# Kernel tuning notes

Hardware: AMD Instinct MI355X
Metric: run time of the kernel (lower is better)

## Reference

```python
import jax, jax.numpy as jnp
import numpy as np

EPS = 1e-6
NUM_HEADS = 12

def _rms(x, w):
    return x * jax.lax.rsqrt(jnp.mean(x * x, axis=-1, keepdims=True) + EPS) * w

def _ln(x, w=None, b=None):
    m = jnp.mean(x, axis=-1, keepdims=True)
    v = jnp.mean((x - m) ** 2, axis=-1, keepdims=True)
    y = (x - m) * jax.lax.rsqrt(v + EPS)
    return y * w + b if w is not None else y

def _rope(x, cos, sin):
    # x: [B,T,H,hd]; cos/sin: [T,hd//2]; adjacent pairs form complex numbers
    B, T, H, hd = x.shape
    xp = x.reshape(B, T, H, hd // 2, 2)
    xr, xi = xp[..., 0], xp[..., 1]
    c = cos[None, :, None, :]
    s = sin[None, :, None, :]
    yr = xr * c - xi * s
    yi = xr * s + xi * c
    return jnp.stack([yr, yi], axis=-1).reshape(B, T, H, hd)

def _attn(q, k, v, mask=None):
    # q: [B,Tq,H,hd], k/v: [B,Tk,H,hd]
    scale = 1.0 / np.sqrt(q.shape[-1]).astype(np.float32)
    s = jnp.einsum('bqhd,bkhd->bhqk', q, k) * scale
    if mask is not None:
        s = jnp.where(mask, s, jnp.asarray(-1e30, s.dtype))
    p = jax.nn.softmax(s, axis=-1)
    return jnp.einsum('bhqk,bkhd->bqhd', p, v)

def _forward(x, context, t_mod, freqs_cos, freqs_sin,
             sa_wq, sa_bq, sa_wk, sa_bk, sa_wv, sa_bv, sa_wo, sa_bo, sa_nq, sa_nk,
             ca_wq, ca_bq, ca_wk, ca_bk, ca_wv, ca_bv, ca_wo, ca_bo, ca_nq, ca_nk,
             norm3_w, norm3_b, ffn_w1, ffn_b1, ffn_w2, ffn_b2, modulation, num_frames):
    B, T, D = x.shape
    F = num_frames
    S = T // F
    H = NUM_HEADS
    hd = D // H
    # adaLN modulation: modulation [1,6,D] broadcast-added to t_mod [B,F,6,D]
    mod = modulation[:, None] + t_mod
    sh_msa, sc_msa, g_msa, sh_mlp, sc_mlp, g_mlp = [mod[:, :, i] for i in range(6)]
    # ---- causal self-attention with RoPE ----
    nx = _ln(x).reshape(B, F, S, D)
    inp = (nx * (1.0 + sc_msa[:, :, None]) + sh_msa[:, :, None]).reshape(B, T, D)
    q = _rms(inp @ sa_wq + sa_bq, sa_nq).reshape(B, T, H, hd)
    k = _rms(inp @ sa_wk + sa_bk, sa_nk).reshape(B, T, H, hd)
    v = (inp @ sa_wv + sa_bv).reshape(B, T, H, hd)
    rq = _rope(q, freqs_cos, freqs_sin)
    rk = _rope(k, freqs_cos, freqs_sin)
    frame_id = jnp.arange(T) // S
    mask = (frame_id[None, :] <= frame_id[:, None])[None, None]  # block-causal by frame
    y = _attn(rq, rk, v, mask).reshape(B, T, D) @ sa_wo + sa_bo
    x = x + (y.reshape(B, F, S, D) * g_msa[:, :, None]).reshape(B, T, D)
    # ---- cross-attention (no image branch) ----
    xn = _ln(x, norm3_w, norm3_b)
    Tc = context.shape[1]
    q = _rms(xn @ ca_wq + ca_bq, ca_nq).reshape(B, T, H, hd)
    k = _rms(context @ ca_wk + ca_bk, ca_nk).reshape(B, Tc, H, hd)
    v = (context @ ca_wv + ca_bv).reshape(B, Tc, H, hd)
    y = _attn(q, k, v).reshape(B, T, D) @ ca_wo + ca_bo
    x = x + y
    # ---- FFN with modulation ----
    nx = _ln(x).reshape(B, F, S, D)
    inp = (nx * (1.0 + sc_mlp[:, :, None]) + sh_mlp[:, :, None]).reshape(B, T, D)
    h = jax.nn.gelu(inp @ ffn_w1 + ffn_b1, approximate=True)
    y = h @ ffn_w2 + ffn_b2
    x = x + (y.reshape(B, F, S, D) * g_mlp[:, :, None]).reshape(B, T, D)
    return x

def setup_inputs() -> dict:
    key = jax.random.key(0)
    B, F, S, D, FF, Tc = 1, 6, 512, 1536, 8960, 512
    T = F * S
    hd = D // NUM_HEADS
    ks = iter(jax.random.split(key, 48))
    def rn(shape, std=1.0):
        return jax.random.normal(next(ks), shape, dtype=jnp.float32) * std
    pos = jnp.arange(T, dtype=jnp.float32)
    inv = 1.0 / (10000.0 ** (jnp.arange(hd // 2, dtype=jnp.float32) / (hd // 2)))
    ang = pos[:, None] * inv[None, :]
    inp = {
        'x': rn((B, T, D)),
        'context': rn((B, Tc, D)),
        't_mod': rn((B, F, 6, D), 0.1),
        'freqs_cos': jnp.cos(ang),
        'freqs_sin': jnp.sin(ang),
    }
    w = 0.02
    for p in ['sa', 'ca']:
        inp[p + '_wq'] = rn((D, D), w); inp[p + '_bq'] = jnp.zeros((D,), jnp.float32)
        inp[p + '_wk'] = rn((D, D), w); inp[p + '_bk'] = jnp.zeros((D,), jnp.float32)
        inp[p + '_wv'] = rn((D, D), w); inp[p + '_bv'] = jnp.zeros((D,), jnp.float32)
        inp[p + '_wo'] = rn((D, D), w); inp[p + '_bo'] = jnp.zeros((D,), jnp.float32)
        inp[p + '_nq'] = jnp.ones((D,), jnp.float32)
        inp[p + '_nk'] = jnp.ones((D,), jnp.float32)
    inp['norm3_w'] = jnp.ones((D,), jnp.float32)
    inp['norm3_b'] = jnp.zeros((D,), jnp.float32)
    inp['ffn_w1'] = rn((D, FF), w); inp['ffn_b1'] = jnp.zeros((FF,), jnp.float32)
    inp['ffn_w2'] = rn((FF, D), w); inp['ffn_b2'] = jnp.zeros((D,), jnp.float32)
    inp['modulation'] = rn((1, 6, D), 1.0 / np.sqrt(D))
    inp['num_frames'] = F
    return inp

def reference(x, context, t_mod, freqs_cos, freqs_sin,
              sa_wq, sa_bq, sa_wk, sa_bk, sa_wv, sa_bv, sa_wo, sa_bo, sa_nq, sa_nk,
              ca_wq, ca_bq, ca_wk, ca_bk, ca_wv, ca_bv, ca_wo, ca_bo, ca_nq, ca_nk,
              norm3_w, norm3_b, ffn_w1, ffn_b1, ffn_w2, ffn_b2, modulation, num_frames):
    return _forward(x, context, t_mod, freqs_cos, freqs_sin,
                    sa_wq, sa_bq, sa_wk, sa_bk, sa_wv, sa_bv, sa_wo, sa_bo, sa_nq, sa_nk,
                    ca_wq, ca_bq, ca_wk, ca_bk, ca_wv, ca_bv, ca_wo, ca_bo, ca_nq, ca_nk,
                    norm3_w, norm3_b, ffn_w1, ffn_b1, ffn_w2, ffn_b2, modulation, num_frames)
```

## Files before the change

kernel.cpp:

```cpp
#include <hip/hip_runtime.h>
#include <cmath>

#define DEV __device__ __forceinline__

constexpr int T_TOK   = 3072;
constexpr int D_MODEL = 1536;
constexpr int FRAMES  = 6;
constexpr int NH      = 12;
constexpr int HD      = 128;
constexpr int FF_DIM  = 8960;
constexpr int TC      = 512;
constexpr float EPS_F = 1e-6f;
constexpr float ATT_SCALE = 0.08838834764831845f;

typedef short bf16x8 __attribute__((ext_vector_type(8)));
typedef float f32x4  __attribute__((ext_vector_type(4)));

DEV ushort f2bf(float f) {
  unsigned u = __builtin_bit_cast(unsigned, f);
  unsigned r = u + 0x7fff + ((u >> 16) & 1);
  return (ushort)(r >> 16);
}

DEV void gload16(const void* g, void* l) {
  __builtin_amdgcn_global_load_lds(
      (const __attribute__((address_space(1))) void*)g,
      (__attribute__((address_space(3))) void*)l, 16, 0, 0);
}

__global__ __launch_bounds__(256) void mod_kernel(
    const float* __restrict__ modulation, const float* __restrict__ t_mod,
    float* __restrict__ modbuf) {
  int i = blockIdx.x * 256 + threadIdx.x;
  if (i >= FRAMES * 6 * D_MODEL) return;
  int d  = i % D_MODEL;
  int mi = (i / D_MODEL) % 6;
  modbuf[i] = modulation[mi * D_MODEL + d] + t_mod[i];
}

__global__ __launch_bounds__(256) void cvt_bf16_kernel(
    const float* __restrict__ in, ushort* __restrict__ out, int n4) {
  int i = blockIdx.x * 256 + threadIdx.x;
  if (i >= n4) return;
  float4 v = ((const float4*)in)[i];
  ushort4 o;
  o.x = f2bf(v.x); o.y = f2bf(v.y); o.z = f2bf(v.z); o.w = f2bf(v.w);
  ((ushort4*)out)[i] = o;
}

__global__ __launch_bounds__(256) void wconv_kernel(
    const float* __restrict__ W, ushort* __restrict__ Wt, int K, int N) {
  __shared__ float tile[64][65];
  const int k0 = blockIdx.y * 64, n0 = blockIdx.x * 64;
  const int t = threadIdx.x;
  const int r = t >> 4, c4 = (t & 15) * 4;
#pragma unroll
  for (int i = 0; i < 4; ++i) {
    float4 v = *(const float4*)&W[(long)(k0 + r + 16 * i) * N + n0 + c4];
    tile[r + 16 * i][c4 + 0] = v.x; tile[r + 16 * i][c4 + 1] = v.y;
    tile[r + 16 * i][c4 + 2] = v.z; tile[r + 16 * i][c4 + 3] = v.w;
  }
  __syncthreads();
  const int orow = t >> 5, oc2 = (t & 31) * 2;
#pragma unroll
  for (int j = 0; j < 8; ++j) {
    int nrow = orow + 8 * j;
    ushort2 o;
    o.x = f2bf(tile[oc2][nrow]);
    o.y = f2bf(tile[oc2 + 1][nrow]);
    *(ushort2*)&Wt[(long)(n0 + nrow) * K + k0 + oc2] = o;
  }
}

__global__ __launch_bounds__(256) void vtrans_kernel(
    const float* __restrict__ V, int stride, int Tv, ushort* __restrict__ Vt) {
  __shared__ float tile[64][65];
  const int t0 = blockIdx.x * 64, d0 = blockIdx.y * 64;
  const int t = threadIdx.x;
  const int r = t >> 4, c4 = (t & 15) * 4;
#pragma unroll
  for (int i = 0; i < 4; ++i) {
    float4 v = *(const float4*)&V[(long)(t0 + r + 16 * i) * stride + d0 + c4];
    tile[r + 16 * i][c4 + 0] = v.x; tile[r + 16 * i][c4 + 1] = v.y;
    tile[r + 16 * i][c4 + 2] = v.z; tile[r + 16 * i][c4 + 3] = v.w;
  }
  __syncthreads();
  const int od = t >> 2, tc = (t & 3) * 16;
#pragma unroll
  for (int j4 = 0; j4 < 4; ++j4) {
    ushort4 o;
    o.x = f2bf(tile[tc + j4 * 4 + 0][od]);
    o.y = f2bf(tile[tc + j4 * 4 + 1][od]);
    o.z = f2bf(tile[tc + j4 * 4 + 2][od]);
    o.w = f2bf(tile[tc + j4 * 4 + 3][od]);
    *(ushort4*)&Vt[(long)(d0 + od) * Tv + t0 + tc + j4 * 4] = o;
  }
}

DEV void block_reduce2(float& s, float& s2, float* red, int t) {
  int lane = t & 63, w = t >> 6;
#pragma unroll
  for (int o = 32; o > 0; o >>= 1) {
    s  += __shfl_down(s,  o, 64);
    s2 += __shfl_down(s2, o, 64);
  }
  if (lane == 0) { red[w] = s; red[4 + w] = s2; }
  __syncthreads();
  s  = (red[0] + red[1]) + (red[2] + red[3]);
  s2 = (red[4] + red[5]) + (red[6] + red[7]);
}

__global__ __launch_bounds__(256) void ln_mod_kernel(
    const float* __restrict__ x, const float* __restrict__ modbuf,
    int ish, int isc, ushort* __restrict__ out) {
  __shared__ float red[8];
  int row = blockIdx.x, t = threadIdx.x;
  const float* xr = x + (long)row * D_MODEL;
  float vals[6];
  float s = 0.f, s2 = 0.f;
#pragma unroll
  for (int i = 0; i < 6; ++i) {
    float v = xr[t + 256 * i];
    vals[i] = v; s += v; s2 += v * v;
  }
  block_reduce2(s, s2, red, t);
  float mean = s * (1.f / D_MODEL);
  float var  = s2 * (1.f / D_MODEL) - mean * mean;
  float rs   = 1.f / sqrtf(var + EPS_F);
  const float* mb = modbuf + (long)(row >> 9) * 6 * D_MODEL;
#pragma unroll
  for (int i = 0; i < 6; ++i) {
    int d = t + 256 * i;
    float y = (vals[i] - mean) * rs;
    out[(long)row * D_MODEL + d] = f2bf(y * (1.f + mb[isc * D_MODEL + d]) + mb[ish * D_MODEL + d]);
  }
}

__global__ __launch_bounds__(256) void ln_affine_kernel(
    const float* __restrict__ x, const float* __restrict__ w,
    const float* __restrict__ b, ushort* __restrict__ out) {
  __shared__ float red[8];
  int row = blockIdx.x, t = threadIdx.x;
  const float* xr = x + (long)row * D_MODEL;
  float vals[6];
  float s = 0.f, s2 = 0.f;
#pragma unroll
  for (int i = 0; i < 6; ++i) {
    float v = xr[t + 256 * i];
    vals[i] = v; s += v; s2 += v * v;
  }
  block_reduce2(s, s2, red, t);
  float mean = s * (1.f / D_MODEL);
  float var  = s2 * (1.f / D_MODEL) - mean * mean;
  float rs   = 1.f / sqrtf(var + EPS_F);
#pragma unroll
  for (int i = 0; i < 6; ++i) {
    int d = t + 256 * i;
    float y = (vals[i] - mean) * rs;
    out[(long)row * D_MODEL + d] = f2bf(y * w[d] + b[d]);
  }
}

template <bool ROPE>
__global__ __launch_bounds__(256) void rmsbf_kernel(
    const float* __restrict__ in, int stride, const float* __restrict__ w,
    const float* __restrict__ cosb, const float* __restrict__ sinb,
    ushort* __restrict__ out) {
  __shared__ float red[8];
  int row = blockIdx.x, t = threadIdx.x;
  const float* xr = in + (long)row * stride;
  float vals[6];
  float s2 = 0.f, dummy = 0.f;
#pragma unroll
  for (int i = 0; i < 6; ++i) {
    float v = xr[t + 256 * i];
    vals[i] = v; s2 += v * v;
  }
  block_reduce2(s2, dummy, red, t);
  float rs = 1.f / sqrtf(s2 * (1.f / D_MODEL) + EPS_F);
  ushort* orow = out + (long)row * D_MODEL;
  if (ROPE) {
#pragma unroll
    for (int pi = 0; pi < 3; ++pi) {
      int p = t + 256 * pi;
      int hh = p >> 6, ii = p & 63;
      int d0 = hh * HD + 2 * ii;
      float a = xr[d0] * rs * w[d0];
      float b = xr[d0 + 1] * rs * w[d0 + 1];
      float c = cosb[(long)row * 64 + ii];
      float sn = sinb[(long)row * 64 + ii];
      ushort2 o;
      o.x = f2bf(a * c - b * sn);
      o.y = f2bf(a * sn + b * c);
      *(ushort2*)&orow[d0] = o;
    }
  } else {
#pragma unroll
    for (int i = 0; i < 6; ++i) {
      int d = t + 256 * i;
      orow[d] = f2bf(vals[i] * rs * w[d]);
    }
  }
}

template <int EPI>
__global__ __launch_bounds__(256) void mgemm_kernel(
    const ushort* __restrict__ A, const ushort* __restrict__ Bt,
    const float* __restrict__ bias, const float* __restrict__ res,
    const float* __restrict__ modbuf, int gidx,
    void* __restrict__ Cout, int M, int N, int K, int ldc) {
  __shared__ ushort As[128 * 32];
  __shared__ ushort Bs[128 * 32];
  const int t = threadIdx.x;
  const int bm = blockIdx.y * 128, bn = blockIdx.x * 128;
  const int wave = t >> 6, lane = t & 63;
  const int wr = (wave >> 1) * 64, wc = (wave & 1) * 64;
  const int l15 = lane & 15, l4 = lane >> 4;

  f32x4 acc[4][4] = {};

  const int srow  = t >> 2;
  const int skoff = (t & 3) * 8;
  const ushort* Ag = A  + (long)(bm + srow) * K + skoff;
  const ushort* Bg = Bt + (long)(bn + srow) * K + skoff;
  ushort* Asl = As + t * 8;
  ushort* Bsl = Bs + t * 8;
  const long half = (long)64 * K;

  for (int k0 = 0; k0 < K; k0 += 32) {
    __syncthreads();
    gload16(Ag + k0, Asl);
    gload16(Ag + k0 + half, Asl + 2048);
    gload16(Bg + k0, Bsl);
    gload16(Bg + k0 + half, Bsl + 2048);
    asm volatile("s_waitcnt vmcnt(0)" ::: "memory");
    __syncthreads();
    bf16x8 af[4], bfr[4];
#pragma unroll
    for (int m = 0; m < 4; ++m)
      af[m] = *(const bf16x8*)&As[(wr + m * 16 + l15) * 32 + l4 * 8];
#pragma unroll
    for (int n = 0; n < 4; ++n)
      bfr[n] = *(const bf16x8*)&Bs[(wc + n * 16 + l15) * 32 + l4 * 8];
#pragma unroll
    for (int m = 0; m < 4; ++m)
#pragma unroll
      for (int n = 0; n < 4; ++n)
        acc[m][n] = __builtin_amdgcn_mfma_f32_16x16x32_bf16(af[m], bfr[n], acc[m][n], 0, 0, 0);
  }

#pragma unroll
  for (int m = 0; m < 4; ++m) {
#pragma unroll
    for (int r = 0; r < 4; ++r) {
      const int grow = bm + wr + m * 16 + l4 * 4 + r;
      const long rowoff = (long)grow * ldc;
      const float* mrow = nullptr;
      if (EPI == 2) mrow = modbuf + (long)((grow >> 9) * 6 + gidx) * D_MODEL;
#pragma unroll
      for (int n = 0; n < 4; ++n) {
        const int gcol = bn + wc + n * 16 + l15;
        float val = acc[m][n][r] + bias[gcol];
        if (EPI == 0) {
          ((float*)Cout)[rowoff + gcol] = val;
        } else if (EPI == 1) {
          float u = val;
          val = u / (1.f + __expf(-1.5957691216057308f * (u + 0.044715f * u * u * u)));
          ((ushort*)Cout)[rowoff + gcol] = f2bf(val);
        } else if (EPI == 2) {
          ((float*)Cout)[rowoff + gcol] = res[rowoff + gcol] + val * mrow[gcol];
        } else {
          ((float*)Cout)[rowoff + gcol] = res[rowoff + gcol] + val;
        }
      }
    }
  }
}

template <bool CAUSAL>
__global__ __launch_bounds__(256) void mattn_kernel(
    const ushort* __restrict__ Qb, const ushort* __restrict__ Kb,
    const ushort* __restrict__ Vt, ushort* __restrict__ O, int Tk) {
  __shared__ ushort Kl[64 * 136];
  __shared__ ushort Vl[128 * 72];
  __shared__ ushort Pl[4][32 * 72];
  const int t = threadIdx.x;
  const int h = blockIdx.y;
  const int qb = CAUSAL ? (gridDim.x - 1 - blockIdx.x) : blockIdx.x;
  const int q0 = qb * 128;
  const int wave = t >> 6, lane = t & 63;
  const int l15 = lane & 15, l4 = lane >> 4;
  const int wq = wave * 32;
  const int kmax = CAUSAL ? (((q0 >> 9) + 1) << 9) : Tk;

  bf16x8 qf[2][4];
#pragma unroll
  for (int mf = 0; mf < 2; ++mf)
#pragma unroll
    for (int ks = 0; ks < 4; ++ks)
      qf[mf][ks] = *(const bf16x8*)&Qb[(long)(q0 + wq + mf * 16 + l15) * D_MODEL + h * HD + ks * 32 + l4 * 8];

  f32x4 ao[2][8] = {};
  float m_run[8], l_run[8];
#pragma unroll
  for (int i = 0; i < 8; ++i) { m_run[i] = -1e30f; l_run[i] = 0.f; }

  const ushort* Vh = Vt + (long)h * HD * Tk;
  ushort* Plw = &Pl[wave][0];

  for (int k0 = 0; k0 < kmax; k0 += 64) {
    __syncthreads();
    {
      const int r = t >> 2, c0 = (t & 3) * 8;
      const ushort* src = Kb + (long)(k0 + r) * D_MODEL + h * HD + c0;
#pragma unroll
      for (int j = 0; j < 4; ++j)
        *(bf16x8*)&Kl[r * 136 + c0 + j * 32] = *(const bf16x8*)&src[j * 32];
    }
    {
      const int d = t >> 1, c0 = (t & 1) * 32;
      const ushort* src = Vh + (long)d * Tk + k0 + c0;
#pragma unroll
      for (int j = 0; j < 4; ++j)
        *(bf16x8*)&Vl[d * 72 + c0 + j * 8] = *(const bf16x8*)&src[j * 8];
    }
    __syncthreads();

    f32x4 s[2][4] = {};
#pragma unroll
    for (int n = 0; n < 4; ++n) {
      bf16x8 kf[4];
#pragma unroll
      for (int ks = 0; ks < 4; ++ks)
        kf[ks] = *(const bf16x8*)&Kl[(n * 16 + l15) * 136 + ks * 32 + l4 * 8];
#pragma unroll
      for (int mf = 0; mf < 2; ++mf)
#pragma unroll
        for (int ks = 0; ks < 4; ++ks)
          s[mf][n] = __builtin_amdgcn_mfma_f32_16x16x32_bf16(qf[mf][ks], kf[ks], s[mf][n], 0, 0, 0);
    }

#pragma unroll
    for (int mf = 0; mf < 2; ++mf) {
      float mx[4], al[4], ps[4];
#pragma unroll
      for (int r = 0; r < 4; ++r)
        mx[r] = fmaxf(fmaxf(s[mf][0][r], s[mf][1][r]), fmaxf(s[mf][2][r], s[mf][3][r])) * ATT_SCALE;
#pragma unroll
      for (int off = 1; off < 16; off <<= 1)
#pragma unroll
        for (int r = 0; r < 4; ++r)
          mx[r] = fmaxf(mx[r], __shfl_xor(mx[r], off, 64));
#pragma unroll
      for (int r = 0; r < 4; ++r) {
        const int idx = mf * 4 + r;
        float mnew = fmaxf(m_run[idx], mx[r]);
        al[r] = __expf(m_run[idx] - mnew);
        m_run[idx] = mnew;
        float p0 = __expf(s[mf][0][r] * ATT_SCALE - mnew);
        float p1 = __expf(s[mf][1][r] * ATT_SCALE - mnew);
        float p2 = __expf(s[mf][2][r] * ATT_SCALE - mnew);
        float p3 = __expf(s[mf][3][r] * ATT_SCALE - mnew);
        s[mf][0][r] = p0; s[mf][1][r] = p1; s[mf][2][r] = p2; s[mf][3][r] = p3;
        ps[r] = (p0 + p1) + (p2 + p3);
      }
#pragma unroll
      for (int off = 1; off < 16; off <<= 1)
#pragma unroll
        for (int r = 0; r < 4; ++r)
          ps[r] += __shfl_xor(ps[r], off, 64);
#pragma unroll
      for (int r = 0; r < 4; ++r)
        l_run[mf * 4 + r] = l_run[mf * 4 + r] * al[r] + ps[r];
#pragma unroll
      for (int nd = 0; nd < 8; ++nd)
#pragma unroll
        for (int r = 0; r < 4; ++r)
          ao[mf][nd][r] *= al[r];
#pragma unroll
      for (int n = 0; n < 4; ++n)
#pragma unroll
        for (int r = 0; r < 4; ++r)
          Plw[(mf * 16 + l4 * 4 + r) * 72 + n * 16 + l15] = f2bf(s[mf][n][r]);
    }

#pragma unroll
    for (int ks2 = 0; ks2 < 2; ++ks2) {
      bf16x8 paf[2];
#pragma unroll
      for (int mf = 0; mf < 2; ++mf)
        paf[mf] = *(const bf16x8*)&Plw[(mf * 16 + l15) * 72 + ks2 * 32 + l4 * 8];
#pragma unroll
      for (int nd = 0; nd < 8; ++nd) {
        bf16x8 vf = *(const bf16x8*)&Vl[(nd * 16 + l15) * 72 + ks2 * 32 + l4 * 8];
#pragma unroll
        for (int mf = 0; mf < 2; ++mf)
          ao[mf][nd] = __builtin_amdgcn_mfma_f32_16x16x32_bf16(paf[mf], vf, ao[mf][nd], 0, 0, 0);
      }
    }
  }

#pragma unroll
  for (int mf = 0; mf < 2; ++mf)
#pragma unroll
    for (int r = 0; r < 4; ++r) {
      float inv = 1.f / l_run[mf * 4 + r];
      long rb = (long)(q0 + wq + mf * 16 + l4 * 4 + r) * D_MODEL + h * HD + l15;
#pragma unroll
      for (int nd = 0; nd < 8; ++nd)
        O[rb + nd * 16] = f2bf(ao[mf][nd][r] * inv);
    }
}

extern "C" void kernel_launch(void* const* d_in, const int* in_sizes, int n_in,
                              void* d_out, int out_size, void* d_ws, size_t ws_size,
                              hipStream_t stream) {
  const float* x      = (const float*)d_in[0];
  const float* ctx    = (const float*)d_in[1];
  const float* t_mod  = (const float*)d_in[2];
  const float* fcos   = (const float*)d_in[3];
  const float* fsin   = (const float*)d_in[4];
  const float* sa_wq = (const float*)d_in[5];  const float* sa_bq = (const float*)d_in[6];
  const float* sa_wk = (const float*)d_in[7];  const float* sa_bk = (const float*)d_in[8];
  const float* sa_wv = (const float*)d_in[9];  const float* sa_bv = (const float*)d_in[10];
  const float* sa_wo = (const float*)d_in[11]; const float* sa_bo = (const float*)d_in[12];
  const float* sa_nq = (const float*)d_in[13]; const float* sa_nk = (const float*)d_in[14];
  const float* ca_wq = (const float*)d_in[15]; const float* ca_bq = (const float*)d_in[16];
  const float* ca_wk = (const float*)d_in[17]; const float* ca_bk = (const float*)d_in[18];
  const float* ca_wv = (const float*)d_in[19]; const float* ca_bv = (const float*)d_in[20];
  const float* ca_wo = (const float*)d_in[21]; const float* ca_bo = (const float*)d_in[22];
  const float* ca_nq = (const float*)d_in[23]; const float* ca_nk = (const float*)d_in[24];
  const float* n3w = (const float*)d_in[25]; const float* n3b = (const float*)d_in[26];
  const float* w1 = (const float*)d_in[27]; const float* b1 = (const float*)d_in[28];
  const float* w2 = (const float*)d_in[29]; const float* b2 = (const float*)d_in[30];
  const float* modulation = (const float*)d_in[31];
  (void)in_sizes; (void)n_in; (void)out_size; (void)ws_size;

  float* out = (float*)d_out;
  char*  wsb = (char*)d_ws;

  float*  modbuf  = (float*)(wsb + 0);
  float*  biascat = (float*)(wsb + 221184);
  ushort* wscr    = (ushort*)(wsb + 251904);
  ushort* inp     = (ushort*)(wsb + 27777024);
  char*   R       = wsb + 37214208;
  ushort* attb    = (ushort*)(wsb + 93837312);
  ushort* Qbb     = (ushort*)(wsb + 103274496);
  char*   KV      = wsb + 112711680;
  char*   M       = wsb + 131586048;

  float*  qkvb = (float*)R;
  float*  qc   = (float*)R;
  float*  kvc  = (float*)(R + 18874368);
  ushort* hb   = (ushort*)R;
  ushort* Kbb  = (ushort*)KV;
  ushort* Vtb  = (ushort*)(KV + 9437184);
  float*  x1   = (float*)KV;
  ushort* ctxb = (ushort*)M;
  ushort* Kbc  = (ushort*)M;
  ushort* Vtc  = (ushort*)(M + 1572864);

  dim3 b256(256);
  dim3 gT(T_TOK);
  dim3 gattn(T_TOK / 128, NH);
  const long WQ = (long)D_MODEL * D_MODEL;

  mod_kernel<<<dim3((FRAMES * 6 * D_MODEL + 255) / 256), b256, 0, stream>>>(modulation, t_mod, modbuf);
  hipMemcpyAsync(biascat + 0,    sa_bq, 6144, hipMemcpyDeviceToDevice, stream);
  hipMemcpyAsync(biascat + 1536, sa_bk, 6144, hipMemcpyDeviceToDevice, stream);
  hipMemcpyAsync(biascat + 3072, sa_bv, 6144, hipMemcpyDeviceToDevice, stream);
  hipMemcpyAsync(biascat + 4608, ca_bk, 6144, hipMemcpyDeviceToDevice, stream);
  hipMemcpyAsync(biascat + 6144, ca_bv, 6144, hipMemcpyDeviceToDevice, stream);
  cvt_bf16_kernel<<<dim3(TC * D_MODEL / 4 / 256), b256, 0, stream>>>(ctx, ctxb, TC * D_MODEL / 4);

  dim3 gw(D_MODEL / 64, D_MODEL / 64);

  ln_mod_kernel<<<gT, b256, 0, stream>>>(x, modbuf, 0, 1, inp);
  wconv_kernel<<<gw, b256, 0, stream>>>(sa_wq, wscr + 0 * WQ, D_MODEL, D_MODEL);
  wconv_kernel<<<gw, b256, 0, stream>>>(sa_wk, wscr + 1 * WQ, D_MODEL, D_MODEL);
  wconv_kernel<<<gw, b256, 0, stream>>>(sa_wv, wscr + 2 * WQ, D_MODEL, D_MODEL);
  mgemm_kernel<0><<<dim3(4608 / 128, T_TOK / 128), b256, 0, stream>>>(
      inp, wscr, biascat, nullptr, nullptr, 0, qkvb, T_TOK, 4608, D_MODEL, 4608);
  rmsbf_kernel<true><<<gT, b256, 0, stream>>>(qkvb, 4608, sa_nq, fcos, fsin, Qbb);
  rmsbf_kernel<true><<<gT, b256, 0, stream>>>(qkvb + 1536, 4608, sa_nk, fcos, fsin, Kbb);
  vtrans_kernel<<<dim3(T_TOK / 64, D_MODEL / 64), b256, 0, stream>>>(qkvb + 3072, 4608, T_TOK, Vtb);
  mattn_kernel<true><<<gattn, b256, 0, stream>>>(Qbb, Kbb, Vtb, attb, T_TOK);
  wconv_kernel<<<gw, b256, 0, stream>>>(sa_wo, wscr, D_MODEL, D_MODEL);
  mgemm_kernel<2><<<dim3(D_MODEL / 128, T_TOK / 128), b256, 0, stream>>>(
      attb, wscr, sa_bo, x, modbuf, 2, x1, T_TOK, D_MODEL, D_MODEL, D_MODEL);

  ln_affine_kernel<<<gT, b256, 0, stream>>>(x1, n3w, n3b, inp);
  wconv_kernel<<<gw, b256, 0, stream>>>(ca_wq, wscr, D_MODEL, D_MODEL);
  mgemm_kernel<0><<<dim3(D_MODEL / 128, T_TOK / 128), b256, 0, stream>>>(
      inp, wscr, ca_bq, nullptr, nullptr, 0, qc, T_TOK, D_MODEL, D_MODEL, D_MODEL);
  rmsbf_kernel<false><<<gT, b256, 0, stream>>>(qc, 1536, ca_nq, nullptr, nullptr, Qbb);
  wconv_kernel<<<gw, b256, 0, stream>>>(ca_wk, wscr + 0 * WQ, D_MODEL, D_MODEL);
  wconv_kernel<<<gw, b256, 0, stream>>>(ca_wv, wscr + 1 * WQ, D_MODEL, D_MODEL);
  mgemm_kernel<0><<<dim3(3072 / 128, TC / 128), b256, 0, stream>>>(
      ctxb, wscr, biascat + 4608, nullptr, nullptr, 0, kvc, TC, 3072, D_MODEL, 3072);
  rmsbf_kernel<false><<<dim3(TC), b256, 0, stream>>>(kvc, 3072, ca_nk, nullptr, nullptr, Kbc);
  vtrans_kernel<<<dim3(TC / 64, D_MODEL / 64), b256, 0, stream>>>(kvc + 1536, 3072, TC, Vtc);
  mattn_kernel<false><<<gattn, b256, 0, stream>>>(Qbb, Kbc, Vtc, attb, TC);
  wconv_kernel<<<gw, b256, 0, stream>>>(ca_wo, wscr, D_MODEL, D_MODEL);
  mgemm_kernel<3><<<dim3(D_MODEL / 128, T_TOK / 128), b256, 0, stream>>>(
      attb, wscr, ca_bo, x1, nullptr, 0, x1, T_TOK, D_MODEL, D_MODEL, D_MODEL);

  ln_mod_kernel<<<gT, b256, 0, stream>>>(x1, modbuf, 3, 4, inp);
  wconv_kernel<<<dim3(FF_DIM / 64, D_MODEL / 64), b256, 0, stream>>>(w1, wscr, D_MODEL, FF_DIM);
  mgemm_kernel<1><<<dim3(FF_DIM / 128, T_TOK / 128), b256, 0, stream>>>(
      inp, wscr, b1, nullptr, nullptr, 0, hb, T_TOK, FF_DIM, D_MODEL, FF_DIM);
  wconv_kernel<<<dim3(D_MODEL / 64, FF_DIM / 64), b256, 0, stream>>>(w2, wscr, FF_DIM, D_MODEL);
  mgemm_kernel<2><<<dim3(D_MODEL / 128, T_TOK / 128), b256, 0, stream>>>(
      hb, wscr, b2, x1, modbuf, 5, out, T_TOK, D_MODEL, FF_DIM, D_MODEL);
}
```

Baseline: 1.235 ms.

## Load attention K/V fragments straight from global and transpose score tile

The attention kernel no longer stages K and V tiles in shared memory behind block barriers. Each wave now loads its K and V MFMA fragments directly from global memory into registers. The score MFMA is computed as K·Q, so each lane holds one query row: the row max and row sum need only two cross-lane shuffles, and the scale is folded into exp2. The 2D grid becomes a 1D grid with a remap intended to spread heads and query blocks across XCDs. The trade-off is that all four waves now fetch the same K/V tiles, which multiplies L2 traffic and raises register pressure.

```diff
diff --git a/kernel.cpp b/kernel.cpp
--- a/kernel.cpp
+++ b/kernel.cpp
@@ -20,6 +20,10 @@
   unsigned u = __builtin_bit_cast(unsigned, f);
   unsigned r = u + 0x7fff + ((u >> 16) & 1);
   return (ushort)(r >> 16);
+}
+
+DEV unsigned packbf2(float lo, float hi) {
+  return (unsigned)f2bf(lo) | ((unsigned)f2bf(hi) << 16);
 }
 
 DEV void gload16(const void* g, void* l) {
@@ -281,17 +285,17 @@
 __global__ __launch_bounds__(256) void mattn_kernel(
     const ushort* __restrict__ Qb, const ushort* __restrict__ Kb,
     const ushort* __restrict__ Vt, ushort* __restrict__ O, int Tk) {
-  __shared__ ushort Kl[64 * 136];
-  __shared__ ushort Vl[128 * 72];
   __shared__ ushort Pl[4][32 * 72];
   const int t = threadIdx.x;
-  const int h = blockIdx.y;
-  const int qb = CAUSAL ? (gridDim.x - 1 - blockIdx.x) : blockIdx.x;
-  const int q0 = qb * 128;
-  const int wave = t >> 6, lane = t & 63;
-  const int l15 = lane & 15, l4 = lane >> 4;
+  const int bid = blockIdx.x;
+  const int L = (bid & 7) * 36 + (bid >> 3);
+  const int h  = L / 24;
+  const int q0 = (23 - (L % 24)) * 128;
+  const int wave = t >> 6;
+  const int l15 = t & 15, l4 = (t >> 4) & 3;
   const int wq = wave * 32;
   const int kmax = CAUSAL ? (((q0 >> 9) + 1) << 9) : Tk;
+  const float SC2 = ATT_SCALE * 1.4426950408889634f;
 
   bf16x8 qf[2][4];
 #pragma unroll
@@ -301,115 +305,105 @@
       qf[mf][ks] = *(const bf16x8*)&Qb[(long)(q0 + wq + mf * 16 + l15) * D_MODEL + h * HD + ks * 32 + l4 * 8];
 
   f32x4 ao[2][8] = {};
-  float m_run[8], l_run[8];
-#pragma unroll
-  for (int i = 0; i < 8; ++i) { m_run[i] = -1e30f; l_run[i] = 0.f; }
-
+  float m_run[2] = {-1e30f, -1e30f};
+  float l_run[2] = {0.f, 0.f};
+
+  const ushort* Kh = Kb + h * HD;
   const ushort* Vh = Vt + (long)h * HD * Tk;
-  ushort* Plw = &Pl[wave][0];
+  ushort*   Plw   = &Pl[wave][0];
+  unsigned* Plw32 = (unsigned*)Plw;
 
   for (int k0 = 0; k0 < kmax; k0 += 64) {
-    __syncthreads();
-    {
-      const int r = t >> 2, c0 = (t & 3) * 8;
-      const ushort* src = Kb + (long)(k0 + r) * D_MODEL + h * HD + c0;
-#pragma unroll
-      for (int j = 0; j < 4; ++j)
-        *(bf16x8*)&Kl[r * 136 + c0 + j * 32] = *(const bf16x8*)&src[j * 32];
+    bf16x8 kf[4][4];
+#pragma unroll
+    for (int n = 0; n < 4; ++n)
+#pragma unroll
+      for (int ks = 0; ks < 4; ++ks)
+        kf[n][ks] = *(const bf16x8*)&Kh[(long)(k0 + n * 16 + l15) * D_MODEL + ks * 32 + l4 * 8];
+
+    f32x4 s[2][4] = {};
+#pragma unroll
+    for (int n = 0; n < 4; ++n)
+#pragma unroll
+      for (int mf = 0; mf < 2; ++mf)
+#pragma unroll
+        for (int ks = 0; ks < 4; ++ks)
+          s[mf][n] = __builtin_amdgcn_mfma_f32_16x16x32_bf16(kf[n][ks], qf[mf][ks], s[mf][n], 0, 0, 0);
+
+    bf16x8 vf[8][2];
+#pragma unroll
+    for (int nd = 0; nd < 8; ++nd)
+#pragma unroll
+      for (int ks2 = 0; ks2 < 2; ++ks2)
+        vf[nd][ks2] = *(const bf16x8*)&Vh[(long)(nd * 16 + l15) * Tk + k0 + ks2 * 32 + l4 * 8];
+
+#pragma unroll
+    for (int mf = 0; mf < 2; ++mf) {
+      float mx = s[mf][0][0];
+#pragma unroll
+      for (int n = 0; n < 4; ++n)
+#pragma unroll
+        for (int r = 0; r < 4; ++r) mx = fmaxf(mx, s[mf][n][r]);
+      mx *= SC2;
+      mx = fmaxf(mx, __shfl_xor(mx, 16, 64));
+      mx = fmaxf(mx, __shfl_xor(mx, 32, 64));
+      float mnew = fmaxf(m_run[mf], mx);
+      float al = exp2f(m_run[mf] - mnew);
+      m_run[mf] = mnew;
+      float p[4][4];
+      float ps = 0.f;
+#pragma unroll
+      for (int n = 0; n < 4; ++n)
+#pragma unroll
+        for (int r = 0; r < 4; ++r) {
+          p[n][r] = exp2f(s[mf][n][r] * SC2 - mnew);
+          ps += p[n][r];
+        }
+      ps += __shfl_xor(ps, 16, 64);
+      ps += __shfl_xor(ps, 32, 64);
+      l_run[mf] = l_run[mf] * al + ps;
+#pragma unroll
+      for (int n = 0; n < 4; ++n) {
+        uint2 wv;
+        wv.x = packbf2(p[n][0], p[n][1]);
+        wv.y = packbf2(p[n][2], p[n][3]);
+        *(uint2*)&Plw32[(mf * 16 + l15) * 36 + n * 8 + l4 * 2] = wv;
+      }
+      float alq[4];
+#pragma unroll
+      for (int r = 0; r < 4; ++r) alq[r] = __shfl(al, l4 * 4 + r, 64);
+#pragma unroll
+      for (int nd = 0; nd < 8; ++nd)
+#pragma unroll
+        for (int r = 0; r < 4; ++r) ao[mf][nd][r] *= alq[r];
     }
-    {
-      const int d = t >> 1, c0 = (t & 1) * 32;
-      const ushort* src = Vh + (long)d * Tk + k0 + c0;
-#pragma unroll
-      for (int j = 0; j < 4; ++j)
-        *(bf16x8*)&Vl[d * 72 + c0 + j * 8] = *(const bf16x8*)&src[j * 8];
+
+    bf16x8 paf[2][2];
+#pragma unroll
+    for (int mf = 0; mf < 2; ++mf)
+#pragma unroll
+      for (int ks2 = 0; ks2 < 2; ++ks2)
+        paf[mf][ks2] = *(const bf16x8*)&Plw[(mf * 16 + l15) * 72 + ks2 * 32 + l4 * 8];
+#pragma unroll
+    for (int nd = 0; nd < 8; ++nd)
+#pragma unroll
+      for (int ks2 = 0; ks2 < 2; ++ks2)
+#pragma unroll
+        for (int mf = 0; mf < 2; ++mf)
+          ao[mf][nd] = __builtin_amdgcn_mfma_f32_16x16x32_bf16(paf[mf][ks2], vf[nd][ks2], ao[mf][nd], 0, 0, 0);
+  }
+
+#pragma unroll
+  for (int mf = 0; mf < 2; ++mf) {
+#pragma unroll
+    for (int r = 0; r < 4; ++r) {
+      float linv = 1.f / __shfl(l_run[mf], l4 * 4 + r, 64);
+      long rb = (long)(q0 + wq + mf * 16 + l4 * 4 + r) * D_MODEL + h * HD + l15;
+#pragma unroll
+      for (int nd = 0; nd < 8; ++nd)
+        O[rb + nd * 16] = f2bf(ao[mf][nd][r] * linv);
     }
-    __syncthreads();
-
-    f32x4 s[2][4] = {};
-#pragma unroll
-    for (int n = 0; n < 4; ++n) {
-      bf16x8 kf[4];
-#pragma unroll
-      for (int ks = 0; ks < 4; ++ks)
-        kf[ks] = *(const bf16x8*)&Kl[(n * 16 + l15) * 136 + ks * 32 + l4 * 8];
-#pragma unroll
-      for (int mf = 0; mf < 2; ++mf)
-#pragma unroll
-        for (int ks = 0; ks < 4; ++ks)
-          s[mf][n] = __builtin_amdgcn_mfma_f32_16x16x32_bf16(qf[mf][ks], kf[ks], s[mf][n], 0, 0, 0);
-    }
-
-#pragma unroll
-    for (int mf = 0; mf < 2; ++mf) {
-      float mx[4], al[4], ps[4];
-#pragma unroll
-      for (int r = 0; r < 4; ++r)
-        mx[r] = fmaxf(fmaxf(s[mf][0][r], s[mf][1][r]), fmaxf(s[mf][2][r], s[mf][3][r])) * ATT_SCALE;
-#pragma unroll
-      for (int off = 1; off < 16; off <<= 1)
-#pragma unroll
-        for (int r = 0; r < 4; ++r)
-          mx[r] = fmaxf(mx[r], __shfl_xor(mx[r], off, 64));
-#pragma unroll
-      for (int r = 0; r < 4; ++r) {
-        const int idx = mf * 4 + r;
-        float mnew = fmaxf(m_run[idx], mx[r]);
-        al[r] = __expf(m_run[idx] - mnew);
-        m_run[idx] = mnew;
-        float p0 = __expf(s[mf][0][r] * ATT_SCALE - mnew);
-        float p1 = __expf(s[mf][1][r] * ATT_SCALE - mnew);
-        float p2 = __expf(s[mf][2][r] * ATT_SCALE - mnew);
-        float p3 = __expf(s[mf][3][r] * ATT_SCALE - mnew);
-        s[mf][0][r] = p0; s[mf][1][r] = p1; s[mf][2][r] = p2; s[mf][3][r] = p3;
-        ps[r] = (p0 + p1) + (p2 + p3);
-      }
-#pragma unroll
-      for (int off = 1; off < 16; off <<= 1)
-#pragma unroll
-        for (int r = 0; r < 4; ++r)
-          ps[r] += __shfl_xor(ps[r], off, 64);
-#pragma unroll
-      for (int r = 0; r < 4; ++r)
-        l_run[mf * 4 + r] = l_run[mf * 4 + r] * al[r] + ps[r];
-#pragma unroll
-      for (int nd = 0; nd < 8; ++nd)
-#pragma unroll
-        for (int r = 0; r < 4; ++r)
-          ao[mf][nd][r] *= al[r];
-#pragma unroll
-      for (int n = 0; n < 4; ++n)
-#pragma unroll
-        for (int r = 0; r < 4; ++r)
-          Plw[(mf * 16 + l4 * 4 + r) * 72 + n * 16 + l15] = f2bf(s[mf][n][r]);
-    }
-
-#pragma unroll
-    for (int ks2 = 0; ks2 < 2; ++ks2) {
-      bf16x8 paf[2];
-#pragma unroll
-      for (int mf = 0; mf < 2; ++mf)
-        paf[mf] = *(const bf16x8*)&Plw[(mf * 16 + l15) * 72 + ks2 * 32 + l4 * 8];
-#pragma unroll
-      for (int nd = 0; nd < 8; ++nd) {
-        bf16x8 vf = *(const bf16x8*)&Vl[(nd * 16 + l15) * 72 + ks2 * 32 + l4 * 8];
-#pragma unroll
-        for (int mf = 0; mf < 2; ++mf)
-          ao[mf][nd] = __builtin_amdgcn_mfma_f32_16x16x32_bf16(paf[mf], vf, ao[mf][nd], 0, 0, 0);
-      }
-    }
-  }
-
-#pragma unroll
-  for (int mf = 0; mf < 2; ++mf)
-#pragma unroll
-    for (int r = 0; r < 4; ++r) {
-      float inv = 1.f / l_run[mf * 4 + r];
-      long rb = (long)(q0 + wq + mf * 16 + l4 * 4 + r) * D_MODEL + h * HD + l15;
-#pragma unroll
-      for (int nd = 0; nd < 8; ++nd)
-        O[rb + nd * 16] = f2bf(ao[mf][nd][r] * inv);
-    }
+  }
 }
 
 extern "C" void kernel_launch(void* const* d_in, const int* in_sizes, int n_in,
@@ -462,7 +456,7 @@
 
   dim3 b256(256);
   dim3 gT(T_TOK);
-  dim3 gattn(T_TOK / 128, NH);
+  dim3 gattn(T_TOK / 128 * NH);
   const long WQ = (long)D_MODEL * D_MODEL;
 
   mod_kernel<<<dim3((FRAMES * 6 * D_MODEL + 255) / 256), b256, 0, stream>>>(modulation, t_mod, modbuf);
```

Result: slower. 1.362 ms (+10.3%).
